# Performance work log

Hardware: AMD Instinct MI355X
Metric: run time of the kernel (lower is better)

## Reference

```python
import jax, jax.numpy as jnp
import numpy as np

E = 8          # num_experts
K = 2          # top-k experts per token
CAP_RATIO = 1.05


def setup_inputs() -> dict:
    key = jax.random.key(0)
    ks = jax.random.split(key, 4)
    B, S, D, H = 2, 2048, 1024, 4096
    x = jax.random.normal(ks[0], (B, S, D), jnp.float32)
    Wg = jax.random.normal(ks[1], (E, D), jnp.float32) * 0.02
    W1 = jax.random.normal(ks[2], (E, D, H), jnp.float32) * 0.02
    b1 = jnp.zeros((E, H), jnp.float32)
    W2 = jax.random.normal(ks[3], (E, H, D), jnp.float32) * 0.02
    b2 = jnp.zeros((E, D), jnp.float32)
    return {"x": x, "Wg": Wg, "W1": W1, "b1": b1, "W2": W2, "b2": b2}


def reference(x, Wg, W1, b1, W2, b2):
    # Eval-mode SparseMoE forward (no router noise, no aux-loss metrics).
    B, S, D = x.shape
    T = B * S
    xf = x.reshape(T, D)

    # --- router: softmax gates + top-k ---
    gates = jax.nn.softmax(xf @ Wg.T, axis=-1)          # [T, E]
    topw, topi = jax.lax.top_k(gates, K)                # [T, K]

    # --- capacity-limited dispatch (slot-major order, matching torch loop) ---
    C = int(round(K * T * CAP_RATIO / E))               # buffer capacity per expert
    e_ord = topi.T.reshape(-1)                          # [K*T] expert id per assignment
    tok_ord = jnp.tile(jnp.arange(T), K)                # [K*T] token id per assignment
    oh = jax.nn.one_hot(e_ord, E, dtype=jnp.int32)      # [K*T, E]
    cnt = jnp.take_along_axis(jnp.cumsum(oh, 0) - oh, e_ord[:, None], 1)[:, 0]
    within = cnt < C                                    # first C arrivals per expert accepted
    pos = jnp.where(within, cnt, C)                     # dropped tokens -> dummy slot C

    # scatter accepted tokens into per-expert buffers [E, C+1, D]
    x_disp = xf[tok_ord]
    buf = jnp.zeros((E, C + 1, D), xf.dtype).at[e_ord, pos].add(x_disp)[:, :C]

    # --- grouped expert MLP (Linear -> exact GELU -> Linear) ---
    h = jax.nn.gelu(jnp.einsum('ecd,edh->ech', buf, W1) + b1[:, None, :],
                    approximate=False)
    y = jnp.einsum('ech,ehd->ecd', h, W2) + b2[:, None, :]  # [E, C, D]

    # --- gather back and weighted combine ---
    y_ord = y[e_ord, jnp.minimum(pos, C - 1)] * within[:, None].astype(y.dtype)
    y_tk = y_ord.reshape(K, T, D).transpose(1, 0, 2)     # [T, K, D]
    cw = topw * within.reshape(K, T).T.astype(topw.dtype)
    out = jnp.einsum('tk,tkd->td', cw, y_tk)
    return out.reshape(B, S, D)
```

## Files before the change

kernel.cpp:

```cpp
#include <hip/hip_runtime.h>

typedef __attribute__((ext_vector_type(8))) __bf16 bf16x8;
typedef __attribute__((ext_vector_type(4))) float f32x4;

constexpr int T  = 4096;
constexpr int Dm = 1024;
constexpr int Hm = 4096;
constexpr int NE = 8;
constexpr int CAP = 1075;
constexpr int CP  = 1152;

static __device__ __forceinline__ unsigned short f2bf(float f) {
  unsigned int u = __float_as_uint(f);
  u += 0x7FFFu + ((u >> 16) & 1u);
  return (unsigned short)(u >> 16);
}

static __device__ __forceinline__ void gload_lds16(const void* g, void* l) {
  __builtin_amdgcn_global_load_lds(
      (const __attribute__((address_space(1))) void*)g,
      (__attribute__((address_space(3))) void*)l, 16, 0, 0);
}

__global__ __launch_bounds__(256) void router_kernel(
    const float* __restrict__ x, const float* __restrict__ Wg,
    int* __restrict__ topi, float* __restrict__ topw) {
  int t = blockIdx.x * 4 + (threadIdx.x >> 6);
  int lane = threadIdx.x & 63;
  const float* xr = x + (size_t)t * Dm;
  float acc[NE];
#pragma unroll
  for (int e = 0; e < NE; ++e) acc[e] = 0.f;
  for (int i = lane * 4; i < Dm; i += 256) {
    float4 xv = *(const float4*)(xr + i);
#pragma unroll
    for (int e = 0; e < NE; ++e) {
      float4 wv = *(const float4*)(Wg + e * Dm + i);
      acc[e] += xv.x * wv.x + xv.y * wv.y + xv.z * wv.z + xv.w * wv.w;
    }
  }
#pragma unroll
  for (int off = 32; off > 0; off >>= 1) {
#pragma unroll
    for (int e = 0; e < NE; ++e) acc[e] += __shfl_xor(acc[e], off, 64);
  }
  if (lane == 0) {
    float mx = acc[0];
#pragma unroll
    for (int e = 1; e < NE; ++e) mx = fmaxf(mx, acc[e]);
    float g[NE];
    float s = 0.f;
#pragma unroll
    for (int e = 0; e < NE; ++e) { g[e] = expf(acc[e] - mx); s += g[e]; }
    int i0 = 0; float v0 = g[0];
#pragma unroll
    for (int e = 1; e < NE; ++e) if (g[e] > v0) { v0 = g[e]; i0 = e; }
    int i1 = -1; float v1 = -1e30f;
#pragma unroll
    for (int e = 0; e < NE; ++e) {
      if (e == i0) continue;
      if (g[e] > v1) { v1 = g[e]; i1 = e; }
    }
    float inv = 1.f / s;
    topi[t * 2] = i0; topi[t * 2 + 1] = i1;
    topw[t * 2] = v0 * inv; topw[t * 2 + 1] = v1 * inv;
  }
}

__global__ __launch_bounds__(1024) void dispatch_scan_kernel(
    const int* __restrict__ topi, int* __restrict__ pos, int* __restrict__ within) {
  __shared__ unsigned long long sc0[1024];
  __shared__ unsigned long long sc1[1024];
  const int tid = threadIdx.x;
  int myE[8];
  unsigned long long w0 = 0, w1 = 0;
#pragma unroll
  for (int j = 0; j < 8; ++j) {
    int a = tid * 8 + j;
    int k = a >> 12;
    int t = a & (T - 1);
    int e = topi[t * 2 + k];
    myE[j] = e;
    unsigned long long inc = 1ULL << (16 * (e & 3));
    if (e < 4) w0 += inc; else w1 += inc;
  }
  const unsigned long long l0 = w0, l1 = w1;
  sc0[tid] = w0; sc1[tid] = w1;
  __syncthreads();
  for (int off = 1; off < 1024; off <<= 1) {
    unsigned long long a0 = 0, a1 = 0;
    if (tid >= off) { a0 = sc0[tid - off]; a1 = sc1[tid - off]; }
    __syncthreads();
    w0 += a0; w1 += a1;
    sc0[tid] = w0; sc1[tid] = w1;
    __syncthreads();
  }
  unsigned long long e0 = w0 - l0, e1 = w1 - l1;
#pragma unroll
  for (int j = 0; j < 8; ++j) {
    int a = tid * 8 + j;
    int e = myE[j];
    int sh = 16 * (e & 3);
    int p;
    if (e < 4) { p = (int)((e0 >> sh) & 0xFFFF); e0 += 1ULL << sh; }
    else       { p = (int)((e1 >> sh) & 0xFFFF); e1 += 1ULL << sh; }
    pos[a] = p;
    within[a] = (p < CAP) ? 1 : 0;
  }
}

__global__ __launch_bounds__(256) void scatter_kernel(
    const float* __restrict__ x, const int* __restrict__ topi,
    const int* __restrict__ pos, const int* __restrict__ within,
    unsigned short* __restrict__ buf) {
  int a = blockIdx.x;
  if (!within[a]) return;
  int k = a >> 12, t = a & (T - 1);
  int e = topi[t * 2 + k];
  int p = pos[a];
  const float* src = x + (size_t)t * Dm;
  unsigned short* dst = buf + ((size_t)e * CP + p) * Dm;
  int i = threadIdx.x * 4;
  float4 v = *(const float4*)(src + i);
  ushort4 o;
  o.x = f2bf(v.x); o.y = f2bf(v.y); o.z = f2bf(v.z); o.w = f2bf(v.w);
  *(ushort4*)(dst + i) = o;
}

__global__ __launch_bounds__(256) void transpose_kernel(
    const float* __restrict__ W, unsigned short* __restrict__ Wt,
    int Kd, int N) {
  __shared__ float tile[64][33];
  const int e = blockIdx.z;
  const int n0 = blockIdx.x * 32;
  const int k0 = blockIdx.y * 64;
  const float* src = W + ((long long)e * Kd + k0) * N + n0;
  const int tid = threadIdx.x;
  const int r = tid >> 3;
  const int c4 = (tid & 7) * 4;
#pragma unroll
  for (int hh = 0; hh < 2; ++hh) {
    float4 v = *(const float4*)(src + (long long)(r + 32 * hh) * N + c4);
    tile[r + 32 * hh][c4] = v.x; tile[r + 32 * hh][c4 + 1] = v.y;
    tile[r + 32 * hh][c4 + 2] = v.z; tile[r + 32 * hh][c4 + 3] = v.w;
  }
  __syncthreads();
  const int n = tid >> 4;
  const int k4 = (tid & 15) * 4;
  unsigned short* dst = Wt + ((long long)e * N + n0) * Kd + k0;
#pragma unroll
  for (int hh = 0; hh < 2; ++hh) {
    int nn = n + 16 * hh;
    ushort4 o;
    o.x = f2bf(tile[k4][nn]);     o.y = f2bf(tile[k4 + 1][nn]);
    o.z = f2bf(tile[k4 + 2][nn]); o.w = f2bf(tile[k4 + 3][nn]);
    *(ushort4*)(dst + (long long)nn * Kd + k4) = o;
  }
}

template <bool GELU, bool OUT_BF16>
__global__ __launch_bounds__(256) void gemm_bt_kernel(
    const unsigned short* __restrict__ Aall, const unsigned short* __restrict__ Btall,
    const float* __restrict__ biasAll, void* __restrict__ OutAll,
    int Kd, int N, long long sA, long long sB, long long sO, int sBias,
    int eb, int nM) {
  __shared__ unsigned short Alds[128 * 64];
  __shared__ unsigned short Blds[128 * 64];

  const int lin = blockIdx.x;
  const int e = lin % eb;
  const int q = lin / eb;
  const int mb = q % nM;
  const int nb = q / nM;

  const unsigned short* A  = Aall  + (long long)e * sA + (long long)mb * 128 * Kd;
  const unsigned short* Bt = Btall + (long long)e * sB + (long long)nb * 128 * Kd;
  const float* bias = biasAll + (long long)e * sBias + nb * 128;

  const int tid = threadIdx.x;
  const int lane = tid & 63;
  const int wid = tid >> 6;
  const int wr = (wid >> 1) * 64;
  const int wc = (wid & 1) * 64;
  const int l15 = lane & 15;
  const int khi = lane >> 4;
  const int swz = lane & 7;

  const int srow = lane >> 3;
  const int sslot = (lane & 7) ^ srow;

  f32x4 acc[4][4];
#pragma unroll
  for (int m = 0; m < 4; ++m)
#pragma unroll
    for (int n = 0; n < 4; ++n) acc[m][n] = (f32x4){0.f, 0.f, 0.f, 0.f};

  const int nK = Kd >> 6;
  for (int kt = 0; kt < nK; ++kt) {
    const int kb = kt << 6;
#pragma unroll
    for (int j = 0; j < 4; ++j) {
      const int c = wid * 4 + j;
      const long long rowg = 8 * c + srow;
      gload_lds16(A  + rowg * Kd + kb + sslot * 8, &Alds[c * 512]);
      gload_lds16(Bt + rowg * Kd + kb + sslot * 8, &Blds[c * 512]);
    }
    __syncthreads();
#pragma unroll
    for (int kk = 0; kk < 2; ++kk) {
      bf16x8 af[4], bfv[4];
#pragma unroll
      for (int m = 0; m < 4; ++m)
        af[m] = *(const bf16x8*)&Alds[(wr + m * 16 + l15) * 64 + (((kk * 4 + khi) ^ swz) << 3)];
#pragma unroll
      for (int n = 0; n < 4; ++n)
        bfv[n] = *(const bf16x8*)&Blds[(wc + n * 16 + l15) * 64 + (((kk * 4 + khi) ^ swz) << 3)];
#pragma unroll
      for (int m = 0; m < 4; ++m)
#pragma unroll
        for (int n = 0; n < 4; ++n)
          acc[m][n] = __builtin_amdgcn_mfma_f32_16x16x32_bf16(af[m], bfv[n], acc[m][n], 0, 0, 0);
    }
    __syncthreads();
  }

  const int crow = khi * 4;
#pragma unroll
  for (int m = 0; m < 4; ++m) {
#pragma unroll
    for (int n = 0; n < 4; ++n) {
      const long long col = (long long)nb * 128 + wc + n * 16 + l15;
      const float bvv = bias[wc + n * 16 + l15];
#pragma unroll
      for (int j = 0; j < 4; ++j) {
        const long long row = (long long)mb * 128 + wr + m * 16 + crow + j;
        float v = acc[m][n][j] + bvv;
        if (GELU) v = 0.5f * v * (1.f + erff(v * 0.70710678118654752f));
        if (OUT_BF16)
          ((unsigned short*)OutAll)[(long long)e * sO + row * N + col] = f2bf(v);
        else
          ((float*)OutAll)[(long long)e * sO + row * N + col] = v;
      }
    }
  }
}

__global__ __launch_bounds__(256) void combine_kernel(
    const float* __restrict__ y, const int* __restrict__ topi,
    const float* __restrict__ topw, const int* __restrict__ pos,
    const int* __restrict__ within, float* __restrict__ out) {
  int t = blockIdx.x;
  int i = threadIdx.x * 4;
  float4 r = {0.f, 0.f, 0.f, 0.f};
#pragma unroll
  for (int k = 0; k < 2; ++k) {
    int a = k * T + t;
    if (within[a]) {
      int e = topi[t * 2 + k];
      int p = pos[a];
      float w = topw[t * 2 + k];
      const float* yr = y + ((size_t)e * CP + p) * Dm;
      float4 v = *(const float4*)(yr + i);
      r.x += w * v.x; r.y += w * v.y; r.z += w * v.z; r.w += w * v.w;
    }
  }
  *(float4*)(out + (size_t)t * Dm + i) = r;
}

extern "C" void kernel_launch(void* const* d_in, const int* in_sizes, int n_in,
                              void* d_out, int out_size, void* d_ws, size_t ws_size,
                              hipStream_t stream) {
  const float* x  = (const float*)d_in[0];
  const float* Wg = (const float*)d_in[1];
  const float* W1 = (const float*)d_in[2];
  const float* b1 = (const float*)d_in[3];
  const float* W2 = (const float*)d_in[4];
  const float* b2 = (const float*)d_in[5];
  float* out = (float*)d_out;

  char* ws = (char*)d_ws;
  const size_t sz_h = (size_t)NE * CP * Hm * 2;
  const size_t sz_y = (size_t)NE * CP * Dm * 4;
  const size_t sz_wt_full = (size_t)NE * Hm * Dm * 2;
  const size_t needA = sz_h + sz_y + sz_wt_full + (size_t)2 * T * 16;
  const int EB = (ws_size >= needA) ? NE : 2;

  unsigned short* h = (unsigned short*)ws;
  char* yreg = ws + sz_h;
  unsigned short* buf = (unsigned short*)yreg;
  float* y = (float*)yreg;
  unsigned short* Wt = (unsigned short*)(ws + sz_h + sz_y);
  char* smallp = ws + sz_h + sz_y + (size_t)EB * Hm * Dm * 2;
  int* topi   = (int*)smallp;
  float* topw = (float*)(topi + 2 * T);
  int* pos    = (int*)(topw + 2 * T);
  int* within = pos + 2 * T;

  router_kernel<<<T / 4, 256, 0, stream>>>(x, Wg, topi, topw);
  dispatch_scan_kernel<<<1, 1024, 0, stream>>>(topi, pos, within);
  scatter_kernel<<<2 * T, 256, 0, stream>>>(x, topi, pos, within, buf);

  const int nM = CP / 128;
  for (int e0 = 0; e0 < NE; e0 += EB) {
    transpose_kernel<<<dim3(Hm / 32, Dm / 64, EB), 256, 0, stream>>>(
        W1 + (size_t)e0 * Dm * Hm, Wt, Dm, Hm);
    gemm_bt_kernel<true, true><<<EB * nM * (Hm / 128), 256, 0, stream>>>(
        buf + (size_t)e0 * CP * Dm, Wt, b1 + (size_t)e0 * Hm,
        (void*)(h + (size_t)e0 * CP * Hm),
        Dm, Hm, (long long)CP * Dm, (long long)Hm * Dm, (long long)CP * Hm, Hm,
        EB, nM);
  }
  for (int e0 = 0; e0 < NE; e0 += EB) {
    transpose_kernel<<<dim3(Dm / 32, Hm / 64, EB), 256, 0, stream>>>(
        W2 + (size_t)e0 * Hm * Dm, Wt, Hm, Dm);
    gemm_bt_kernel<false, false><<<EB * nM * (Dm / 128), 256, 0, stream>>>(
        h + (size_t)e0 * CP * Hm, Wt, b2 + (size_t)e0 * Dm,
        (void*)(y + (size_t)e0 * CP * Dm),
        Hm, Dm, (long long)CP * Hm, (long long)Dm * Hm, (long long)CP * Dm, Dm,
        EB, nM);
  }

  combine_kernel<<<T, 256, 0, stream>>>(y, topi, topw, pos, within, out);
}
```

Measured before the change: 344.1 us.

## Fuse weight transposes into router and GEMM1 launches to overlap independent work

Merges the W1 transpose blocks into the router launch, and the W2 transpose blocks into the first expert GEMM launch, using block-index dispatch within a single grid. With enough workspace, both transposed weight buffers are kept separately so W2's transpose can run concurrently with GEMM1. The goal is fewer launches and filling idle CUs with independent memory-bound transpose work during compute-bound phases. It needs extra workspace for a second transposed weight buffer, and heterogeneous blocks in one grid may contend for resources or reduce the GEMM's occupancy.

```diff
diff --git a/kernel.cpp b/kernel.cpp
--- a/kernel.cpp
+++ b/kernel.cpp
@@ -22,10 +22,38 @@
       (__attribute__((address_space(3))) void*)l, 16, 0, 0);
 }
 
-__global__ __launch_bounds__(256) void router_kernel(
+
+static __device__ __forceinline__ void transpose_body(
+    float (*tile)[33], const float* __restrict__ W, unsigned short* __restrict__ Wt,
+    int Kd, int N, int e, int n0, int k0) {
+  const float* src = W + ((long long)e * Kd + k0) * N + n0;
+  const int tid = threadIdx.x;
+  const int r = tid >> 3;
+  const int c4 = (tid & 7) * 4;
+#pragma unroll
+  for (int hh = 0; hh < 2; ++hh) {
+    float4 v = *(const float4*)(src + (long long)(r + 32 * hh) * N + c4);
+    tile[r + 32 * hh][c4] = v.x; tile[r + 32 * hh][c4 + 1] = v.y;
+    tile[r + 32 * hh][c4 + 2] = v.z; tile[r + 32 * hh][c4 + 3] = v.w;
+  }
+  __syncthreads();
+  const int n = tid >> 4;
+  const int k4 = (tid & 15) * 4;
+  unsigned short* dst = Wt + ((long long)e * N + n0) * Kd + k0;
+#pragma unroll
+  for (int hh = 0; hh < 2; ++hh) {
+    int nn = n + 16 * hh;
+    ushort4 o;
+    o.x = f2bf(tile[k4][nn]);     o.y = f2bf(tile[k4 + 1][nn]);
+    o.z = f2bf(tile[k4 + 2][nn]); o.w = f2bf(tile[k4 + 3][nn]);
+    *(ushort4*)(dst + (long long)nn * Kd + k4) = o;
+  }
+}
+
+static __device__ __forceinline__ void router_body(
     const float* __restrict__ x, const float* __restrict__ Wg,
-    int* __restrict__ topi, float* __restrict__ topw) {
-  int t = blockIdx.x * 4 + (threadIdx.x >> 6);
+    int* __restrict__ topi, float* __restrict__ topw, int blk) {
+  int t = blk * 4 + (threadIdx.x >> 6);
   int lane = threadIdx.x & 63;
   const float* xr = x + (size_t)t * Dm;
   float acc[NE];
@@ -65,6 +93,106 @@
     topi[t * 2] = i0; topi[t * 2 + 1] = i1;
     topw[t * 2] = v0 * inv; topw[t * 2 + 1] = v1 * inv;
   }
+}
+
+template <bool GELU, bool OUT_BF16>
+static __device__ __forceinline__ void gemm_body(
+    unsigned short* Alds, unsigned short* Blds,
+    const unsigned short* __restrict__ A, const unsigned short* __restrict__ Bt,
+    const float* __restrict__ bias, void* __restrict__ Out,
+    int Kd, int N, int mb, int nb) {
+  const unsigned short* Ab  = A  + (long long)mb * 128 * Kd;
+  const unsigned short* Btb = Bt + (long long)nb * 128 * Kd;
+
+  const int tid = threadIdx.x;
+  const int lane = tid & 63;
+  const int wid = tid >> 6;
+  const int wr = (wid >> 1) * 64;
+  const int wc = (wid & 1) * 64;
+  const int l15 = lane & 15;
+  const int khi = lane >> 4;
+  const int swz = lane & 7;
+  const int srow = lane >> 3;
+  const int sslot = (lane & 7) ^ srow;
+
+  f32x4 acc[4][4];
+#pragma unroll
+  for (int m = 0; m < 4; ++m)
+#pragma unroll
+    for (int n = 0; n < 4; ++n) acc[m][n] = (f32x4){0.f, 0.f, 0.f, 0.f};
+
+  const int nK = Kd >> 6;
+  for (int kt = 0; kt < nK; ++kt) {
+    const int kb = kt << 6;
+#pragma unroll
+    for (int j = 0; j < 4; ++j) {
+      const int c = wid * 4 + j;
+      const long long rowg = 8 * c + srow;
+      gload_lds16(Ab  + rowg * Kd + kb + sslot * 8, &Alds[c * 512]);
+      gload_lds16(Btb + rowg * Kd + kb + sslot * 8, &Blds[c * 512]);
+    }
+    __syncthreads();
+#pragma unroll
+    for (int kk = 0; kk < 2; ++kk) {
+      bf16x8 af[4], bfv[4];
+#pragma unroll
+      for (int m = 0; m < 4; ++m)
+        af[m] = *(const bf16x8*)&Alds[(wr + m * 16 + l15) * 64 + (((kk * 4 + khi) ^ swz) << 3)];
+#pragma unroll
+      for (int n = 0; n < 4; ++n)
+        bfv[n] = *(const bf16x8*)&Blds[(wc + n * 16 + l15) * 64 + (((kk * 4 + khi) ^ swz) << 3)];
+#pragma unroll
+      for (int m = 0; m < 4; ++m)
+#pragma unroll
+        for (int n = 0; n < 4; ++n)
+          acc[m][n] = __builtin_amdgcn_mfma_f32_16x16x32_bf16(af[m], bfv[n], acc[m][n], 0, 0, 0);
+    }
+    __syncthreads();
+  }
+
+  const int crow = khi * 4;
+#pragma unroll
+  for (int m = 0; m < 4; ++m) {
+#pragma unroll
+    for (int n = 0; n < 4; ++n) {
+      const long long col = (long long)nb * 128 + wc + n * 16 + l15;
+      const float bvv = bias[nb * 128 + wc + n * 16 + l15];
+#pragma unroll
+      for (int j = 0; j < 4; ++j) {
+        const long long row = (long long)mb * 128 + wr + m * 16 + crow + j;
+        float v = acc[m][n][j] + bvv;
+        if (GELU) v = 0.5f * v * (1.f + erff(v * 0.70710678118654752f));
+        if (OUT_BF16)
+          ((unsigned short*)Out)[row * N + col] = f2bf(v);
+        else
+          ((float*)Out)[row * N + col] = v;
+      }
+    }
+  }
+}
+
+
+__global__ __launch_bounds__(256) void router_w1t_kernel(
+    const float* __restrict__ x, const float* __restrict__ Wg,
+    int* __restrict__ topi, float* __restrict__ topw,
+    const float* __restrict__ W1, unsigned short* __restrict__ W1t, int nT) {
+  __shared__ __align__(16) float tile[64][33];
+  const int bid = blockIdx.x;
+  if (bid < nT) {
+    int nb = bid % (Hm / 32);
+    int rest = bid / (Hm / 32);
+    int kb = rest % (Dm / 64);
+    int e = rest / (Dm / 64);
+    transpose_body(tile, W1, W1t, Dm, Hm, e, nb * 32, kb * 64);
+  } else {
+    router_body(x, Wg, topi, topw, bid - nT);
+  }
+}
+
+__global__ __launch_bounds__(256) void transpose_kernel(
+    const float* __restrict__ W, unsigned short* __restrict__ Wt, int Kd, int N) {
+  __shared__ __align__(16) float tile[64][33];
+  transpose_body(tile, W, Wt, Kd, N, blockIdx.z, blockIdx.x * 32, blockIdx.y * 64);
 }
 
 __global__ __launch_bounds__(1024) void dispatch_scan_kernel(
@@ -127,34 +255,30 @@
   *(ushort4*)(dst + i) = o;
 }
 
-__global__ __launch_bounds__(256) void transpose_kernel(
-    const float* __restrict__ W, unsigned short* __restrict__ Wt,
-    int Kd, int N) {
-  __shared__ float tile[64][33];
-  const int e = blockIdx.z;
-  const int n0 = blockIdx.x * 32;
-  const int k0 = blockIdx.y * 64;
-  const float* src = W + ((long long)e * Kd + k0) * N + n0;
-  const int tid = threadIdx.x;
-  const int r = tid >> 3;
-  const int c4 = (tid & 7) * 4;
-#pragma unroll
-  for (int hh = 0; hh < 2; ++hh) {
-    float4 v = *(const float4*)(src + (long long)(r + 32 * hh) * N + c4);
-    tile[r + 32 * hh][c4] = v.x; tile[r + 32 * hh][c4 + 1] = v.y;
-    tile[r + 32 * hh][c4 + 2] = v.z; tile[r + 32 * hh][c4 + 3] = v.w;
-  }
-  __syncthreads();
-  const int n = tid >> 4;
-  const int k4 = (tid & 15) * 4;
-  unsigned short* dst = Wt + ((long long)e * N + n0) * Kd + k0;
-#pragma unroll
-  for (int hh = 0; hh < 2; ++hh) {
-    int nn = n + 16 * hh;
-    ushort4 o;
-    o.x = f2bf(tile[k4][nn]);     o.y = f2bf(tile[k4 + 1][nn]);
-    o.z = f2bf(tile[k4 + 2][nn]); o.w = f2bf(tile[k4 + 3][nn]);
-    *(ushort4*)(dst + (long long)nn * Kd + k4) = o;
+__global__ __launch_bounds__(256) void gemm1_w2t_kernel(
+    const unsigned short* __restrict__ buf, const unsigned short* __restrict__ W1t,
+    const float* __restrict__ b1, unsigned short* __restrict__ h,
+    const float* __restrict__ W2, unsigned short* __restrict__ W2t, int nGemm) {
+  __shared__ __align__(16) char smem[32768];
+  const int bid = blockIdx.x;
+  if (bid < nGemm) {
+    unsigned short* Alds = (unsigned short*)smem;
+    unsigned short* Blds = (unsigned short*)(smem + 16384);
+    const int e = bid & 7;
+    const int q = bid >> 3;
+    const int mb = q % (CP / 128);
+    const int nb = q / (CP / 128);
+    gemm_body<true, true>(Alds, Blds,
+        buf + (size_t)e * CP * Dm, W1t + (size_t)e * Hm * Dm, b1 + (size_t)e * Hm,
+        (void*)(h + (size_t)e * CP * Hm), Dm, Hm, mb, nb);
+  } else {
+    float (*tile)[33] = (float(*)[33])smem;
+    int tb = bid - nGemm;
+    int nb = tb % (Dm / 32);
+    int rest = tb / (Dm / 32);
+    int kb = rest % (Hm / 64);
+    int e = rest / (Hm / 64);
+    transpose_body(tile, W2, W2t, Hm, Dm, e, nb * 32, kb * 64);
   }
 }
 
@@ -164,85 +288,18 @@
     const float* __restrict__ biasAll, void* __restrict__ OutAll,
     int Kd, int N, long long sA, long long sB, long long sO, int sBias,
     int eb, int nM) {
-  __shared__ unsigned short Alds[128 * 64];
-  __shared__ unsigned short Blds[128 * 64];
-
+  __shared__ __align__(16) char smem[32768];
+  unsigned short* Alds = (unsigned short*)smem;
+  unsigned short* Blds = (unsigned short*)(smem + 16384);
   const int lin = blockIdx.x;
   const int e = lin % eb;
   const int q = lin / eb;
   const int mb = q % nM;
   const int nb = q / nM;
-
-  const unsigned short* A  = Aall  + (long long)e * sA + (long long)mb * 128 * Kd;
-  const unsigned short* Bt = Btall + (long long)e * sB + (long long)nb * 128 * Kd;
-  const float* bias = biasAll + (long long)e * sBias + nb * 128;
-
-  const int tid = threadIdx.x;
-  const int lane = tid & 63;
-  const int wid = tid >> 6;
-  const int wr = (wid >> 1) * 64;
-  const int wc = (wid & 1) * 64;
-  const int l15 = lane & 15;
-  const int khi = lane >> 4;
-  const int swz = lane & 7;
-
-  const int srow = lane >> 3;
-  const int sslot = (lane & 7) ^ srow;
-
-  f32x4 acc[4][4];
-#pragma unroll
-  for (int m = 0; m < 4; ++m)
-#pragma unroll
-    for (int n = 0; n < 4; ++n) acc[m][n] = (f32x4){0.f, 0.f, 0.f, 0.f};
-
-  const int nK = Kd >> 6;
-  for (int kt = 0; kt < nK; ++kt) {
-    const int kb = kt << 6;
-#pragma unroll
-    for (int j = 0; j < 4; ++j) {
-      const int c = wid * 4 + j;
-      const long long rowg = 8 * c + srow;
-      gload_lds16(A  + rowg * Kd + kb + sslot * 8, &Alds[c * 512]);
-      gload_lds16(Bt + rowg * Kd + kb + sslot * 8, &Blds[c * 512]);
-    }
-    __syncthreads();
-#pragma unroll
-    for (int kk = 0; kk < 2; ++kk) {
-      bf16x8 af[4], bfv[4];
-#pragma unroll
-      for (int m = 0; m < 4; ++m)
-        af[m] = *(const bf16x8*)&Alds[(wr + m * 16 + l15) * 64 + (((kk * 4 + khi) ^ swz) << 3)];
-#pragma unroll
-      for (int n = 0; n < 4; ++n)
-        bfv[n] = *(const bf16x8*)&Blds[(wc + n * 16 + l15) * 64 + (((kk * 4 + khi) ^ swz) << 3)];
-#pragma unroll
-      for (int m = 0; m < 4; ++m)
-#pragma unroll
-        for (int n = 0; n < 4; ++n)
-          acc[m][n] = __builtin_amdgcn_mfma_f32_16x16x32_bf16(af[m], bfv[n], acc[m][n], 0, 0, 0);
-    }
-    __syncthreads();
-  }
-
-  const int crow = khi * 4;
-#pragma unroll
-  for (int m = 0; m < 4; ++m) {
-#pragma unroll
-    for (int n = 0; n < 4; ++n) {
-      const long long col = (long long)nb * 128 + wc + n * 16 + l15;
-      const float bvv = bias[wc + n * 16 + l15];
-#pragma unroll
-      for (int j = 0; j < 4; ++j) {
-        const long long row = (long long)mb * 128 + wr + m * 16 + crow + j;
-        float v = acc[m][n][j] + bvv;
-        if (GELU) v = 0.5f * v * (1.f + erff(v * 0.70710678118654752f));
-        if (OUT_BF16)
-          ((unsigned short*)OutAll)[(long long)e * sO + row * N + col] = f2bf(v);
-        else
-          ((float*)OutAll)[(long long)e * sO + row * N + col] = v;
-      }
-    }
-  }
+  char* Out = (char*)OutAll + (long long)e * sO * (OUT_BF16 ? 2 : 4);
+  gemm_body<GELU, OUT_BF16>(Alds, Blds,
+      Aall + (long long)e * sA, Btall + (long long)e * sB,
+      biasAll + (long long)e * sBias, (void*)Out, Kd, N, mb, nb);
 }
 
 __global__ __launch_bounds__(256) void combine_kernel(
@@ -281,43 +338,65 @@
   char* ws = (char*)d_ws;
   const size_t sz_h = (size_t)NE * CP * Hm * 2;
   const size_t sz_y = (size_t)NE * CP * Dm * 4;
-  const size_t sz_wt_full = (size_t)NE * Hm * Dm * 2;
-  const size_t needA = sz_h + sz_y + sz_wt_full + (size_t)2 * T * 16;
-  const int EB = (ws_size >= needA) ? NE : 2;
+  const size_t sz_w = (size_t)NE * Hm * Dm * 2;
+  const size_t sz_small = (size_t)2 * T * 16;
+  const size_t need_full = sz_h + sz_y + 2 * sz_w + sz_small;
+  const size_t need_mid  = sz_h + sz_y + sz_w + sz_small;
 
   unsigned short* h = (unsigned short*)ws;
   char* yreg = ws + sz_h;
   unsigned short* buf = (unsigned short*)yreg;
   float* y = (float*)yreg;
-  unsigned short* Wt = (unsigned short*)(ws + sz_h + sz_y);
-  char* smallp = ws + sz_h + sz_y + (size_t)EB * Hm * Dm * 2;
+  unsigned short* W1t = (unsigned short*)(ws + sz_h + sz_y);
+  const bool full = (ws_size >= need_full);
+  const bool mid  = (ws_size >= need_mid);
+  unsigned short* W2t = full ? (W1t + sz_w / 2) : W1t;
+  char* smallp = ws + sz_h + sz_y + (full ? 2 * sz_w : (mid ? sz_w : (size_t)2 * Hm * Dm * 2));
   int* topi   = (int*)smallp;
   float* topw = (float*)(topi + 2 * T);
   int* pos    = (int*)(topw + 2 * T);
   int* within = pos + 2 * T;
 
-  router_kernel<<<T / 4, 256, 0, stream>>>(x, Wg, topi, topw);
-  dispatch_scan_kernel<<<1, 1024, 0, stream>>>(topi, pos, within);
-  scatter_kernel<<<2 * T, 256, 0, stream>>>(x, topi, pos, within, buf);
-
   const int nM = CP / 128;
-  for (int e0 = 0; e0 < NE; e0 += EB) {
-    transpose_kernel<<<dim3(Hm / 32, Dm / 64, EB), 256, 0, stream>>>(
-        W1 + (size_t)e0 * Dm * Hm, Wt, Dm, Hm);
-    gemm_bt_kernel<true, true><<<EB * nM * (Hm / 128), 256, 0, stream>>>(
-        buf + (size_t)e0 * CP * Dm, Wt, b1 + (size_t)e0 * Hm,
-        (void*)(h + (size_t)e0 * CP * Hm),
-        Dm, Hm, (long long)CP * Dm, (long long)Hm * Dm, (long long)CP * Hm, Hm,
-        EB, nM);
-  }
-  for (int e0 = 0; e0 < NE; e0 += EB) {
-    transpose_kernel<<<dim3(Dm / 32, Hm / 64, EB), 256, 0, stream>>>(
-        W2 + (size_t)e0 * Hm * Dm, Wt, Hm, Dm);
-    gemm_bt_kernel<false, false><<<EB * nM * (Dm / 128), 256, 0, stream>>>(
-        h + (size_t)e0 * CP * Hm, Wt, b2 + (size_t)e0 * Dm,
-        (void*)(y + (size_t)e0 * CP * Dm),
-        Hm, Dm, (long long)CP * Hm, (long long)Dm * Hm, (long long)CP * Dm, Dm,
-        EB, nM);
+  const int nT = (Hm / 32) * (Dm / 64) * NE;
+
+  if (mid) {
+    router_w1t_kernel<<<nT + T / 4, 256, 0, stream>>>(x, Wg, topi, topw, W1, W1t, nT);
+    dispatch_scan_kernel<<<1, 1024, 0, stream>>>(topi, pos, within);
+    scatter_kernel<<<2 * T, 256, 0, stream>>>(x, topi, pos, within, buf);
+
+    const int nGemm1 = NE * nM * (Hm / 128);
+    if (full) {
+      gemm1_w2t_kernel<<<nGemm1 + nT, 256, 0, stream>>>(buf, W1t, b1, h, W2, W2t, nGemm1);
+    } else {
+      gemm_bt_kernel<true, true><<<nGemm1, 256, 0, stream>>>(
+          buf, W1t, b1, (void*)h, Dm, Hm,
+          (long long)CP * Dm, (long long)Hm * Dm, (long long)CP * Hm, Hm, NE, nM);
+      transpose_kernel<<<dim3(Dm / 32, Hm / 64, NE), 256, 0, stream>>>(W2, W2t, Hm, Dm);
+    }
+    gemm_bt_kernel<false, false><<<NE * nM * (Dm / 128), 256, 0, stream>>>(
+        h, W2t, b2, (void*)y, Hm, Dm,
+        (long long)CP * Hm, (long long)Dm * Hm, (long long)CP * Dm, Dm, NE, nM);
+  } else {
+    router_w1t_kernel<<<T / 4, 256, 0, stream>>>(x, Wg, topi, topw, W1, W1t, 0);
+    dispatch_scan_kernel<<<1, 1024, 0, stream>>>(topi, pos, within);
+    scatter_kernel<<<2 * T, 256, 0, stream>>>(x, topi, pos, within, buf);
+    for (int e0 = 0; e0 < NE; e0 += 2) {
+      transpose_kernel<<<dim3(Hm / 32, Dm / 64, 2), 256, 0, stream>>>(
+          W1 + (size_t)e0 * Dm * Hm, W1t, Dm, Hm);
+      gemm_bt_kernel<true, true><<<2 * nM * (Hm / 128), 256, 0, stream>>>(
+          buf + (size_t)e0 * CP * Dm, W1t, b1 + (size_t)e0 * Hm,
+          (void*)(h + (size_t)e0 * CP * Hm), Dm, Hm,
+          (long long)CP * Dm, (long long)Hm * Dm, (long long)CP * Hm, Hm, 2, nM);
+    }
+    for (int e0 = 0; e0 < NE; e0 += 2) {
+      transpose_kernel<<<dim3(Dm / 32, Hm / 64, 2), 256, 0, stream>>>(
+          W2 + (size_t)e0 * Hm * Dm, W1t, Hm, Dm);
+      gemm_bt_kernel<false, false><<<2 * nM * (Dm / 128), 256, 0, stream>>>(
+          h + (size_t)e0 * CP * Hm, W1t, b2 + (size_t)e0 * Dm,
+          (void*)(y + (size_t)e0 * CP * Dm), Hm, Dm,
+          (long long)CP * Hm, (long long)Dm * Hm, (long long)CP * Dm, Dm, 2, nM);
+    }
   }
 
   combine_kernel<<<T, 256, 0, stream>>>(y, topi, topw, pos, within, out);
```

Result: slower. 367.7 us (+6.9%).
